# Optimization experiments

Hardware: AMD Instinct MI355X
Metric: run time of the kernel (lower is better)

Reference implementation:

```python
import jax, jax.numpy as jnp
import numpy as np

B, L, D, S = 8, 512, 64, 8


def setup_inputs() -> dict:
    key = jax.random.key(0)
    ks = jax.random.split(key, 8)
    return {
        "lstm1": jax.random.normal(ks[0], (B, L, D), dtype=jnp.float32),
        "lstm2": jax.random.normal(ks[1], (B, L, D), dtype=jnp.float32),
        "W": jax.random.normal(ks[2], (S, D, D), dtype=jnp.float32) * 0.1,
        "V": jax.random.normal(ks[3], (S, 2 * D), dtype=jnp.float32) * 0.1,
        "b": jax.random.normal(ks[4], (S,), dtype=jnp.float32) * 0.1,
        "W_g": jax.random.normal(ks[5], (S, 2 * D), dtype=jnp.float32) * 0.1,
        "b_g": jax.random.normal(ks[6], (S,), dtype=jnp.float32) * 0.1,
        "u": jax.random.normal(ks[7], (1, S), dtype=jnp.float32) * 0.1,
    }


def reference(lstm1, lstm2, W, V, b, W_g, b_g, u):
    # lstm1/lstm2: (B, L, D). Pairwise slot (i, j) pairs lstm1[:, i] with lstm2[:, j].
    d = lstm1.shape[-1]
    # Bilinear tensor-network score: x1_i W_s x2_j -> (B, L, L, S)
    result_w = jnp.einsum('bid,sde,bje->bijs', lstm1, W, lstm2)
    # concat(x1_i, x2_j) @ V^T decomposed to avoid materializing (B,L,L,2D)
    v1 = jnp.einsum('bid,sd->bis', lstm1, V[:, :d])[:, :, None, :]   # (B,L,1,S)
    v2 = jnp.einsum('bjd,sd->bjs', lstm2, V[:, d:])[:, None, :, :]   # (B,1,L,S)
    result_v = v1 + v2                                               # (B,L,L,S)
    g1 = jnp.einsum('bid,sd->bis', lstm1, W_g[:, :d])[:, :, None, :]
    g2 = jnp.einsum('bjd,sd->bjs', lstm2, W_g[:, d:])[:, None, :, :]
    gate = jax.nn.sigmoid(g1 + g2 + b_g)                             # (B,L,L,S)
    result_final = gate * result_w + (1.0 - gate) * jax.nn.sigmoid(result_v) + b
    # Reduce slices with u (shape (1,S)) -> (B,L,L), then add singleton channel dim.
    out = jnp.einsum('bijs,ks->bijk', result_final, u)[..., 0]
    return out[:, None, :, :]  # (B, 1, L, L)
```

## Files before the change

kernel.cpp:

```cpp
#include <hip/hip_runtime.h>
#include <math.h>

typedef float f32x4 __attribute__((ext_vector_type(4)));
typedef short bf16x8 __attribute__((ext_vector_type(8)));

namespace {
constexpr int kB = 8, kL = 512, kD = 64, kS = 8;
constexpr int LP = 72;
constexpr size_t SCL_OFF = 0;
constexpr size_t WT_OFF  = (size_t)4 * 8 * 8 * 512 * 4;
}

__device__ __forceinline__ unsigned short f2bf(float f) {
    unsigned u = __float_as_uint(f);
    u += 0x7FFFu + ((u >> 16) & 1u);
    return (unsigned short)(u >> 16);
}
__device__ __forceinline__ unsigned pk2(float lo, float hi) {
    return (unsigned)f2bf(lo) | ((unsigned)f2bf(hi) << 16);
}

__global__ __launch_bounds__(256) void grn_prep(
    const float* __restrict__ lstm1, const float* __restrict__ lstm2,
    const float* __restrict__ W, const float* __restrict__ V,
    const float* __restrict__ Wg, unsigned char* __restrict__ ws)
{
    float* scl = (float*)(ws + SCL_OFF);
    unsigned short* wt = (unsigned short*)(ws + WT_OFF);
    const int tid = threadIdx.x;
    if (blockIdx.x < 8) {
        const int s = blockIdx.x;
        __shared__ float wsm[64][68];
        const float* pw = W + s * 4096;
        const int row = tid >> 2, c0 = (tid & 3) * 16;
        #pragma unroll
        for (int q = 0; q < 4; q++)
            *(float4*)&wsm[row][c0 + q * 4] = *(const float4*)(pw + row * 64 + c0 + q * 4);
        __syncthreads();
        const int e = tid >> 2, d0 = (tid & 3) * 16;
        unsigned wd[8];
        #pragma unroll
        for (int q = 0; q < 8; q++)
            wd[q] = pk2(wsm[d0 + 2 * q][e], wsm[d0 + 2 * q + 1][e]);
        unsigned short* dst = wt + s * 4096 + e * 64 + d0;
        uint4 a = {wd[0], wd[1], wd[2], wd[3]};
        uint4 c = {wd[4], wd[5], wd[6], wd[7]};
        *(uint4*)(dst) = a;
        *(uint4*)(dst + 8) = c;
    } else {
        const int rb = blockIdx.x - 8;
        const int b = rb >> 3, r0 = (rb & 7) * 64;
        const int kind = tid & 3, row = r0 + (tid >> 2);
        const float* x = (kind < 2 ? lstm1 : lstm2) + ((size_t)b * kL + row) * kD;
        float xr[64];
        #pragma unroll
        for (int q = 0; q < 16; q++)
            *(float4*)&xr[q * 4] = *(const float4*)(x + q * 4);
        const float* vb = (kind & 1 ? Wg : V) + ((kind >> 1) ? kD : 0);
        #pragma unroll
        for (int s = 0; s < kS; s++) {
            const float* vec = vb + s * 2 * kD;
            float a = 0.f;
            #pragma unroll
            for (int q = 0; q < 16; q++) {
                const float4 vv = *(const float4*)(vec + q * 4);
                a = fmaf(vv.x, xr[q * 4 + 0], a);
                a = fmaf(vv.y, xr[q * 4 + 1], a);
                a = fmaf(vv.z, xr[q * 4 + 2], a);
                a = fmaf(vv.w, xr[q * 4 + 3], a);
            }
            scl[(((size_t)kind * 8 + b) * 8 + s) * 512 + row] = a;
        }
    }
}

__device__ __forceinline__ void load_wb(
    bf16x8 WB[4][2], const unsigned short* __restrict__ wt, int s, int fr, int fh)
{
    #pragma unroll
    for (int ne = 0; ne < 4; ne++)
        #pragma unroll
        for (int kb = 0; kb < 2; kb++)
            WB[ne][kb] = *(const bf16x8*)(wt + s * 4096 + (ne * 16 + fr) * 64
                                          + fh * 8 + kb * 32);
}

__device__ __forceinline__ void grn_body(
    const bf16x8 WB[4][2], const bf16x8 A1[2][2], const bf16x8 Bf[2][2],
    unsigned short (*__restrict__ tsw)[LP], const float scl[4][kS][64],
    float oacc[2][2][4], int s, int fr, int fh, int wm, int wn,
    float us, float bgs)
{
    #pragma unroll
    for (int mb = 0; mb < 2; mb++)
        #pragma unroll
        for (int ne = 0; ne < 4; ne++) {
            f32x4 z = {0.f, 0.f, 0.f, 0.f};
            f32x4 t = __builtin_amdgcn_mfma_f32_16x16x32_bf16(A1[mb][0], WB[ne][0], z, 0, 0, 0);
            t = __builtin_amdgcn_mfma_f32_16x16x32_bf16(A1[mb][1], WB[ne][1], t, 0, 0, 0);
            #pragma unroll
            for (int r = 0; r < 4; r++)
                tsw[mb * 16 + fh * 4 + r][ne * 16 + fr] = f2bf(t[r]);
        }
    bf16x8 At[2][2];
    #pragma unroll
    for (int mb = 0; mb < 2; mb++)
        #pragma unroll
        for (int kb = 0; kb < 2; kb++)
            At[mb][kb] = *(const bf16x8*)&tsw[mb * 16 + fr][fh * 8 + kb * 32];
    #pragma unroll
    for (int mb = 0; mb < 2; mb++)
        #pragma unroll
        for (int nb = 0; nb < 2; nb++) {
            f32x4 z = {0.f, 0.f, 0.f, 0.f};
            f32x4 acc = __builtin_amdgcn_mfma_f32_16x16x32_bf16(At[mb][0], Bf[nb][0], z, 0, 0, 0);
            acc = __builtin_amdgcn_mfma_f32_16x16x32_bf16(At[mb][1], Bf[nb][1], acc, 0, 0, 0);
            const int jj = wn * 32 + nb * 16 + fr;
            const float v2 = scl[2][s][jj], g2 = scl[3][s][jj];
            #pragma unroll
            for (int r = 0; r < 4; r++) {
                const int ii = wm * 32 + mb * 16 + fh * 4 + r;
                const float v1 = scl[0][s][ii], g1 = scl[1][s][ii];
                const float gate = 1.f / (1.f + __expf(-(g1 + g2 + bgs)));
                const float sv = 1.f / (1.f + __expf(-(v1 + v2)));
                const float res = fmaf(gate, acc[r] - sv, sv);
                oacc[mb][nb][r] = fmaf(us, res, oacc[mb][nb][r]);
            }
        }
}

__global__ __launch_bounds__(256, 2) void grn_fusedm(
    const float* __restrict__ lstm1, const float* __restrict__ lstm2,
    const float* __restrict__ bS, const float* __restrict__ bg,
    const float* __restrict__ u, const unsigned char* __restrict__ ws,
    float* __restrict__ out)
{
    const float* sclw = (const float*)(ws + SCL_OFF);
    const unsigned short* wt = (const unsigned short*)(ws + WT_OFF);
    const int jt = blockIdx.x, it = blockIdx.y, b = blockIdx.z;
    __shared__ __align__(16) unsigned short x1t[64][LP];
    __shared__ __align__(16) unsigned short x2t[64][LP];
    __shared__ __align__(16) unsigned short ts[4][32][LP];
    __shared__ float scl[4][kS][64];
    const int tid = threadIdx.x;
    {
        const float* p1 = lstm1 + ((size_t)b * kL + it * 64) * kD;
        const float* p2 = lstm2 + ((size_t)b * kL + jt * 64) * kD;
        const int row = tid >> 2, c0 = (tid & 3) * 16;
        unsigned w1[8], w2[8];
        #pragma unroll
        for (int q = 0; q < 4; q++) {
            const float4 a = *(const float4*)(p1 + row * 64 + c0 + q * 4);
            const float4 c = *(const float4*)(p2 + row * 64 + c0 + q * 4);
            w1[q * 2] = pk2(a.x, a.y); w1[q * 2 + 1] = pk2(a.z, a.w);
            w2[q * 2] = pk2(c.x, c.y); w2[q * 2 + 1] = pk2(c.z, c.w);
        }
        uint4 a0 = {w1[0], w1[1], w1[2], w1[3]}, a1 = {w1[4], w1[5], w1[6], w1[7]};
        uint4 c0v = {w2[0], w2[1], w2[2], w2[3]}, c1 = {w2[4], w2[5], w2[6], w2[7]};
        *(uint4*)&x1t[row][c0] = a0; *(uint4*)&x1t[row][c0 + 8] = a1;
        *(uint4*)&x2t[row][c0] = c0v; *(uint4*)&x2t[row][c0 + 8] = c1;
    }
    {
        const int p0 = tid * 8, kind = p0 >> 9, rem = p0 & 511, s = rem >> 6, cc = rem & 63;
        const int base = (kind < 2 ? it : jt) * 64;
        const float* g = sclw + (((size_t)kind * 8 + b) * 8 + s) * 512 + base + cc;
        *(float4*)&scl[kind][s][cc] = *(const float4*)g;
        *(float4*)&scl[kind][s][cc + 4] = *(const float4*)(g + 4);
    }
    __syncthreads();
    const int lane = tid & 63, w = tid >> 6;
    const int wm = w >> 1, wn = w & 1;
    const int fr = lane & 15, fh = lane >> 4;
    unsigned short (*__restrict__ tsw)[LP] = ts[w];
    bf16x8 A1[2][2], Bf[2][2];
    #pragma unroll
    for (int mb = 0; mb < 2; mb++)
        #pragma unroll
        for (int kb = 0; kb < 2; kb++)
            A1[mb][kb] = *(const bf16x8*)&x1t[wm * 32 + mb * 16 + fr][fh * 8 + kb * 32];
    #pragma unroll
    for (int nb = 0; nb < 2; nb++)
        #pragma unroll
        for (int kb = 0; kb < 2; kb++)
            Bf[nb][kb] = *(const bf16x8*)&x2t[wn * 32 + nb * 16 + fr][fh * 8 + kb * 32];
    float ur[kS], bgr[kS];
    #pragma unroll
    for (int s = 0; s < kS; s++) { ur[s] = u[s]; bgr[s] = bS[s]; }
    float bias_c = 0.f;
    #pragma unroll
    for (int s = 0; s < kS; s++) bias_c = fmaf(ur[s], bgr[s], bias_c);
    #pragma unroll
    for (int s = 0; s < kS; s++) bgr[s] = bg[s];
    float oacc[2][2][4];
    #pragma unroll
    for (int mb = 0; mb < 2; mb++)
        #pragma unroll
        for (int nb = 0; nb < 2; nb++)
            #pragma unroll
            for (int r = 0; r < 4; r++) oacc[mb][nb][r] = bias_c;

    bf16x8 WBa[4][2], WBb[4][2];
    load_wb(WBa, wt, 0, fr, fh);
    #pragma unroll 1
    for (int s = 0; s < kS; s += 2) {
        load_wb(WBb, wt, s + 1, fr, fh);
        grn_body(WBa, A1, Bf, tsw, scl, oacc, s, fr, fh, wm, wn, ur[s], bgr[s]);
        load_wb(WBa, wt, (s + 2) & 7, fr, fh);
        grn_body(WBb, A1, Bf, tsw, scl, oacc, s + 1, fr, fh, wm, wn, ur[s + 1], bgr[s + 1]);
    }
    float* op = out + ((size_t)b * kL + it * 64) * kL + jt * 64;
    #pragma unroll
    for (int mb = 0; mb < 2; mb++)
        #pragma unroll
        for (int nb = 0; nb < 2; nb++)
            #pragma unroll
            for (int r = 0; r < 4; r++)
                op[(wm * 32 + mb * 16 + fh * 4 + r) * kL + wn * 32 + nb * 16 + fr]
                    = oacc[mb][nb][r];
}

extern "C" void kernel_launch(void* const* d_in, const int* in_sizes, int n_in,
                              void* d_out, int out_size, void* d_ws, size_t ws_size,
                              hipStream_t stream) {
    const float* lstm1 = (const float*)d_in[0];
    const float* lstm2 = (const float*)d_in[1];
    const float* W     = (const float*)d_in[2];
    const float* V     = (const float*)d_in[3];
    const float* bS    = (const float*)d_in[4];
    const float* Wg    = (const float*)d_in[5];
    const float* bg    = (const float*)d_in[6];
    const float* u     = (const float*)d_in[7];
    unsigned char* ws = (unsigned char*)d_ws;
    grn_prep<<<72, 256, 0, stream>>>(lstm1, lstm2, W, V, Wg, ws);
    grn_fusedm<<<dim3(kL / 64, kL / 64, kB), 256, 0, stream>>>(
        lstm1, lstm2, bS, bg, u, ws, (float*)d_out);
}
```

Measured before the change: 112.7 us.

## Fold prep kernel into main kernel, computing projections and W conversion per block

Removes the separate prep launch. Each block now computes its own V/W_g projections for its 64-row tiles, and converts W from fp32 to bf16 on the fly with strided scalar loads. This saves a launch and the workspace round-trip. In exchange, the projection FMAs are repeated across the 8 tiles that share each row, W is reloaded as uncoalesced scalar fp32 reads in every block, and the double-buffered W prefetch is dropped.

```diff
diff --git a/kernel.cpp b/kernel.cpp
--- a/kernel.cpp
+++ b/kernel.cpp
@@ -7,8 +7,6 @@
 namespace {
 constexpr int kB = 8, kL = 512, kD = 64, kS = 8;
 constexpr int LP = 72;
-constexpr size_t SCL_OFF = 0;
-constexpr size_t WT_OFF  = (size_t)4 * 8 * 8 * 512 * 4;
 }
 
 __device__ __forceinline__ unsigned short f2bf(float f) {
@@ -20,69 +18,22 @@
     return (unsigned)f2bf(lo) | ((unsigned)f2bf(hi) << 16);
 }
 
-__global__ __launch_bounds__(256) void grn_prep(
-    const float* __restrict__ lstm1, const float* __restrict__ lstm2,
-    const float* __restrict__ W, const float* __restrict__ V,
-    const float* __restrict__ Wg, unsigned char* __restrict__ ws)
+__device__ __forceinline__ void load_wb_direct(
+    bf16x8 WB[4][2], const float* __restrict__ Wv, int s, int fr, int fh)
 {
-    float* scl = (float*)(ws + SCL_OFF);
-    unsigned short* wt = (unsigned short*)(ws + WT_OFF);
-    const int tid = threadIdx.x;
-    if (blockIdx.x < 8) {
-        const int s = blockIdx.x;
-        __shared__ float wsm[64][68];
-        const float* pw = W + s * 4096;
-        const int row = tid >> 2, c0 = (tid & 3) * 16;
-        #pragma unroll
-        for (int q = 0; q < 4; q++)
-            *(float4*)&wsm[row][c0 + q * 4] = *(const float4*)(pw + row * 64 + c0 + q * 4);
-        __syncthreads();
-        const int e = tid >> 2, d0 = (tid & 3) * 16;
-        unsigned wd[8];
-        #pragma unroll
-        for (int q = 0; q < 8; q++)
-            wd[q] = pk2(wsm[d0 + 2 * q][e], wsm[d0 + 2 * q + 1][e]);
-        unsigned short* dst = wt + s * 4096 + e * 64 + d0;
-        uint4 a = {wd[0], wd[1], wd[2], wd[3]};
-        uint4 c = {wd[4], wd[5], wd[6], wd[7]};
-        *(uint4*)(dst) = a;
-        *(uint4*)(dst + 8) = c;
-    } else {
-        const int rb = blockIdx.x - 8;
-        const int b = rb >> 3, r0 = (rb & 7) * 64;
-        const int kind = tid & 3, row = r0 + (tid >> 2);
-        const float* x = (kind < 2 ? lstm1 : lstm2) + ((size_t)b * kL + row) * kD;
-        float xr[64];
-        #pragma unroll
-        for (int q = 0; q < 16; q++)
-            *(float4*)&xr[q * 4] = *(const float4*)(x + q * 4);
-        const float* vb = (kind & 1 ? Wg : V) + ((kind >> 1) ? kD : 0);
-        #pragma unroll
-        for (int s = 0; s < kS; s++) {
-            const float* vec = vb + s * 2 * kD;
-            float a = 0.f;
-            #pragma unroll
-            for (int q = 0; q < 16; q++) {
-                const float4 vv = *(const float4*)(vec + q * 4);
-                a = fmaf(vv.x, xr[q * 4 + 0], a);
-                a = fmaf(vv.y, xr[q * 4 + 1], a);
-                a = fmaf(vv.z, xr[q * 4 + 2], a);
-                a = fmaf(vv.w, xr[q * 4 + 3], a);
-            }
-            scl[(((size_t)kind * 8 + b) * 8 + s) * 512 + row] = a;
-        }
-    }
-}
-
-__device__ __forceinline__ void load_wb(
-    bf16x8 WB[4][2], const unsigned short* __restrict__ wt, int s, int fr, int fh)
-{
+    const float* base = Wv + s * 4096 + fh * 8 * 64 + fr;
     #pragma unroll
     for (int ne = 0; ne < 4; ne++)
         #pragma unroll
-        for (int kb = 0; kb < 2; kb++)
-            WB[ne][kb] = *(const bf16x8*)(wt + s * 4096 + (ne * 16 + fr) * 64
-                                          + fh * 8 + kb * 32);
+        for (int kb = 0; kb < 2; kb++) {
+            const float* p = base + kb * 32 * 64 + ne * 16;
+            union { bf16x8 v; uint4 q; } cv;
+            cv.q.x = pk2(p[0 * 64], p[1 * 64]);
+            cv.q.y = pk2(p[2 * 64], p[3 * 64]);
+            cv.q.z = pk2(p[4 * 64], p[5 * 64]);
+            cv.q.w = pk2(p[6 * 64], p[7 * 64]);
+            WB[ne][kb] = cv.v;
+        }
 }
 
 __device__ __forceinline__ void grn_body(
@@ -129,14 +80,13 @@
         }
 }
 
-__global__ __launch_bounds__(256, 2) void grn_fusedm(
+__global__ __launch_bounds__(256, 2) void grn_one(
     const float* __restrict__ lstm1, const float* __restrict__ lstm2,
-    const float* __restrict__ bS, const float* __restrict__ bg,
-    const float* __restrict__ u, const unsigned char* __restrict__ ws,
+    const float* __restrict__ W, const float* __restrict__ V,
+    const float* __restrict__ bS, const float* __restrict__ Wg,
+    const float* __restrict__ bg, const float* __restrict__ u,
     float* __restrict__ out)
 {
-    const float* sclw = (const float*)(ws + SCL_OFF);
-    const unsigned short* wt = (const unsigned short*)(ws + WT_OFF);
     const int jt = blockIdx.x, it = blockIdx.y, b = blockIdx.z;
     __shared__ __align__(16) unsigned short x1t[64][LP];
     __shared__ __align__(16) unsigned short x2t[64][LP];
@@ -161,11 +111,29 @@
         *(uint4*)&x2t[row][c0] = c0v; *(uint4*)&x2t[row][c0 + 8] = c1;
     }
     {
-        const int p0 = tid * 8, kind = p0 >> 9, rem = p0 & 511, s = rem >> 6, cc = rem & 63;
-        const int base = (kind < 2 ? it : jt) * 64;
-        const float* g = sclw + (((size_t)kind * 8 + b) * 8 + s) * 512 + base + cc;
-        *(float4*)&scl[kind][s][cc] = *(const float4*)g;
-        *(float4*)&scl[kind][s][cc + 4] = *(const float4*)(g + 4);
+        const int kind = tid >> 6, row = tid & 63;
+        const float* xr = (kind < 2)
+            ? (lstm1 + ((size_t)b * kL + it * 64 + row) * kD)
+            : (lstm2 + ((size_t)b * kL + jt * 64 + row) * kD);
+        float x[64];
+        #pragma unroll
+        for (int q = 0; q < 16; q++)
+            *(float4*)&x[q * 4] = *(const float4*)(xr + q * 4);
+        const float* vb = ((kind & 1) ? Wg : V) + ((kind & 2) ? kD : 0);
+        #pragma unroll
+        for (int s = 0; s < kS; s++) {
+            const float* vec = vb + s * 2 * kD;
+            float a = 0.f;
+            #pragma unroll
+            for (int q = 0; q < 16; q++) {
+                const float4 vv = *(const float4*)(vec + q * 4);
+                a = fmaf(vv.x, x[q * 4 + 0], a);
+                a = fmaf(vv.y, x[q * 4 + 1], a);
+                a = fmaf(vv.z, x[q * 4 + 2], a);
+                a = fmaf(vv.w, x[q * 4 + 3], a);
+            }
+            scl[kind][s][row] = a;
+        }
     }
     __syncthreads();
     const int lane = tid & 63, w = tid >> 6;
@@ -183,14 +151,9 @@
         #pragma unroll
         for (int kb = 0; kb < 2; kb++)
             Bf[nb][kb] = *(const bf16x8*)&x2t[wn * 32 + nb * 16 + fr][fh * 8 + kb * 32];
-    float ur[kS], bgr[kS];
-    #pragma unroll
-    for (int s = 0; s < kS; s++) { ur[s] = u[s]; bgr[s] = bS[s]; }
     float bias_c = 0.f;
     #pragma unroll
-    for (int s = 0; s < kS; s++) bias_c = fmaf(ur[s], bgr[s], bias_c);
-    #pragma unroll
-    for (int s = 0; s < kS; s++) bgr[s] = bg[s];
+    for (int s = 0; s < kS; s++) bias_c = fmaf(u[s], bS[s], bias_c);
     float oacc[2][2][4];
     #pragma unroll
     for (int mb = 0; mb < 2; mb++)
@@ -199,14 +162,12 @@
             #pragma unroll
             for (int r = 0; r < 4; r++) oacc[mb][nb][r] = bias_c;
 
-    bf16x8 WBa[4][2], WBb[4][2];
-    load_wb(WBa, wt, 0, fr, fh);
     #pragma unroll 1
-    for (int s = 0; s < kS; s += 2) {
-        load_wb(WBb, wt, s + 1, fr, fh);
-        grn_body(WBa, A1, Bf, tsw, scl, oacc, s, fr, fh, wm, wn, ur[s], bgr[s]);
-        load_wb(WBa, wt, (s + 2) & 7, fr, fh);
-        grn_body(WBb, A1, Bf, tsw, scl, oacc, s + 1, fr, fh, wm, wn, ur[s + 1], bgr[s + 1]);
+    for (int s = 0; s < kS; s++) {
+        bf16x8 WB[4][2];
+        load_wb_direct(WB, W, s, fr, fh);
+        const float us = u[s], bgs = bg[s];
+        grn_body(WB, A1, Bf, tsw, scl, oacc, s, fr, fh, wm, wn, us, bgs);
     }
     float* op = out + ((size_t)b * kL + it * 64) * kL + jt * 64;
     #pragma unroll
@@ -230,8 +191,6 @@
     const float* Wg    = (const float*)d_in[5];
     const float* bg    = (const float*)d_in[6];
     const float* u     = (const float*)d_in[7];
-    unsigned char* ws = (unsigned char*)d_ws;
-    grn_prep<<<72, 256, 0, stream>>>(lstm1, lstm2, W, V, Wg, ws);
-    grn_fusedm<<<dim3(kL / 64, kL / 64, kB), 256, 0, stream>>>(
-        lstm1, lstm2, bS, bg, u, ws, (float*)d_out);
+    grn_one<<<dim3(kL / 64, kL / 64, kB), 256, 0, stream>>>(
+        lstm1, lstm2, W, V, bS, Wg, bg, u, (float*)d_out);
 }
```

New measurement: 133.3 us. 1.18x slower.
